# Kernel tuning notes

Hardware: AMD Instinct MI355X
Metric: run time of the kernel (lower is better)

## Reference

```python
import jax, jax.numpy as jnp
import numpy as np

N, F = 16384, 32
H1, H2, D1, D2 = 64, 64, 32, 1


def setup_inputs() -> dict:
    key = jax.random.key(0)
    ks = jax.random.split(key, 10)
    x = jax.random.normal(ks[0], (N, F), dtype=jnp.float32)
    # pre-normalized adjacency (GCNConv expects D^-1/2 A D^-1/2); mimic with uniform/N
    a = jax.random.uniform(ks[1], (N, N), dtype=jnp.float32) / N
    # glorot-ish scaled params
    W1 = jax.random.normal(ks[2], (F, H1), dtype=jnp.float32) * (1.0 / np.sqrt(F))
    b1 = jnp.zeros((H1,), dtype=jnp.float32)
    W2 = jax.random.normal(ks[3], (H1, H2), dtype=jnp.float32) * (1.0 / np.sqrt(H1))
    b2 = jnp.zeros((H2,), dtype=jnp.float32)
    Wd1 = jax.random.normal(ks[4], (H2, D1), dtype=jnp.float32) * (1.0 / np.sqrt(H2))
    bd1 = jnp.zeros((D1,), dtype=jnp.float32)
    Wd2 = jax.random.normal(ks[5], (D1, D2), dtype=jnp.float32) * (1.0 / np.sqrt(D1))
    bd2 = jnp.zeros((D2,), dtype=jnp.float32)
    return {"x": x, "a": a, "W1": W1, "b1": b1, "W2": W2, "b2": b2,
            "Wd1": Wd1, "bd1": bd1, "Wd2": Wd2, "bd2": bd2}


def reference(x, a, W1, b1, W2, b2, Wd1, bd1, Wd2, bd2):
    # GCNConv: relu(a @ (x @ W) + b)   (a is pre-normalized)
    g1 = jax.nn.relu(a @ (x @ W1) + b1)   # [N, 64]
    g2 = jax.nn.relu(a @ (g1 @ W2) + b2)  # [N, 64]
    d3 = jax.nn.relu(g2 @ Wd1 + bd1)      # [N, 32]
    return d3 @ Wd2 + bd2                 # [N, 1]
```

## Files before the change

kernel.cpp:

```cpp
#include <hip/hip_runtime.h>
#include <hip/hip_bf16.h>


typedef __bf16 bf16x8 __attribute__((ext_vector_type(8)));
typedef float  f32x16 __attribute__((ext_vector_type(16)));
typedef float  f32x4v __attribute__((ext_vector_type(4)));
typedef int    i32x4  __attribute__((ext_vector_type(4)));

#define NNODE 16384
#define KDIM  16384
#define HCOL  64

__device__ inline i32x4 pack8(f32x4v a, f32x4v b){
  bf16x8 t;
  t[0]=(__bf16)a[0]; t[1]=(__bf16)a[1]; t[2]=(__bf16)a[2]; t[3]=(__bf16)a[3];
  t[4]=(__bf16)b[0]; t[5]=(__bf16)b[1]; t[6]=(__bf16)b[2]; t[7]=(__bf16)b[3];
  return __builtin_bit_cast(i32x4, t);
}
#define BC(x) __builtin_bit_cast(bf16x8, x)

__global__ __launch_bounds__(256, 1) void gcn_layer_kernel(
    const float* __restrict__ A,
    const __bf16* __restrict__ Ht,
    const float* __restrict__ bias,
    float* __restrict__ G)
{
  __shared__ i32x4 sA[4*2*512];
  __shared__ i32x4 sH[4*2*512];

  const int tid  = threadIdx.x;
  const int lane = tid & 63;
  const int kw   = tid >> 6;
  const int row0 = blockIdx.x * 64;

  const int rA0  = lane >> 3;
  const int ccA  = lane & 7;
  const int swzA = ccA ^ rA0;
  const int r    = lane & 31;
  const int hsub = lane >> 5;
  const int xs   = r & 7;

  const size_t k0 = (size_t)kw * 4096;

  f32x4v ra[16]; i32x4 rh[8];

  const float* pA0 = A + (size_t)(row0 + rA0) * KDIM + k0 + (size_t)ccA*8;
  const i32x4* pH0 = (const i32x4*)Ht + (size_t)rA0 * (KDIM/8) + k0/8 + ccA;

  auto stage_load = [&](int t){
    const float* pA = pA0 + (size_t)t*64;
    #pragma unroll
    for (int pi=0; pi<8; ++pi){
      const float* p = pA + (size_t)pi*8*KDIM;
      ra[2*pi]   = *(const f32x4v*)p;
      ra[2*pi+1] = *(const f32x4v*)(p+4);
    }
    const i32x4* pH = pH0 + (size_t)t*8;
    #pragma unroll
    for (int pi=0; pi<8; ++pi)
      rh[pi] = pH[(size_t)pi*8*(KDIM/8)];
  };

  auto stage_write = [&](int buf){
    i32x4* dA = &sA[(kw*2+buf)*512];
    #pragma unroll
    for (int pi=0; pi<8; ++pi)
      dA[(rA0 + pi*8)*8 + swzA] = pack8(ra[2*pi], ra[2*pi+1]);
    i32x4* dH = &sH[(kw*2+buf)*512];
    #pragma unroll
    for (int pi=0; pi<8; ++pi)
      dH[(rA0 + pi*8)*8 + swzA] = rh[pi];
  };

  f32x16 acc00 = {}, acc01 = {}, acc10 = {}, acc11 = {};

  auto compute = [&](int buf){
    const i32x4* bA = &sA[(kw*2+buf)*512];
    const i32x4* bH = &sH[(kw*2+buf)*512];
    #pragma unroll
    for (int kk=0; kk<4; ++kk){
      int c = (kk*2 + hsub) ^ xs;
      bf16x8 a0 = BC(bA[r*8 + c]);
      bf16x8 a1 = BC(bA[(r+32)*8 + c]);
      bf16x8 b0 = BC(bH[r*8 + c]);
      bf16x8 b1 = BC(bH[(r+32)*8 + c]);
      acc00 = __builtin_amdgcn_mfma_f32_32x32x16_bf16(a0, b0, acc00, 0,0,0);
      acc01 = __builtin_amdgcn_mfma_f32_32x32x16_bf16(a0, b1, acc01, 0,0,0);
      acc10 = __builtin_amdgcn_mfma_f32_32x32x16_bf16(a1, b0, acc10, 0,0,0);
      acc11 = __builtin_amdgcn_mfma_f32_32x32x16_bf16(a1, b1, acc11, 0,0,0);
    }
  };

  stage_load(0);
  stage_write(0);
  stage_load(1);
  #pragma unroll 1
  for (int t=0; t<63; ++t){
    compute(t&1);
    stage_write((t+1)&1);
    if (t < 62) stage_load(t+2);
  }
  compute(1);

  __syncthreads();

  float* red = (float*)sA;
  if (kw > 0){
    float* rd = red + (size_t)(kw-1)*4096;
    #pragma unroll
    for (int j=0; j<16; ++j){
      int rr = (j&3) + 8*(j>>2) + 4*hsub;
      rd[(rr   )*64 + r]      = acc00[j];
      rd[(rr   )*64 + 32 + r] = acc01[j];
      rd[(rr+32)*64 + r]      = acc10[j];
      rd[(rr+32)*64 + 32 + r] = acc11[j];
    }
  }
  __syncthreads();
  if (kw == 0){
    #pragma unroll
    for (int j=0; j<16; ++j){
      int rr = (j&3) + 8*(j>>2) + 4*hsub;
      float v00 = acc00[j] + red[(rr   )*64+r]    + red[4096+(rr   )*64+r]    + red[8192+(rr   )*64+r]    + bias[r];
      float v01 = acc01[j] + red[(rr   )*64+32+r] + red[4096+(rr   )*64+32+r] + red[8192+(rr   )*64+32+r] + bias[32+r];
      float v10 = acc10[j] + red[(rr+32)*64+r]    + red[4096+(rr+32)*64+r]    + red[8192+(rr+32)*64+r]    + bias[r];
      float v11 = acc11[j] + red[(rr+32)*64+32+r] + red[4096+(rr+32)*64+32+r] + red[8192+(rr+32)*64+32+r] + bias[32+r];
      G[(size_t)(row0 + rr     )*HCOL + r]      = fmaxf(v00, 0.f);
      G[(size_t)(row0 + rr     )*HCOL + 32 + r] = fmaxf(v01, 0.f);
      G[(size_t)(row0 + rr + 32)*HCOL + r]      = fmaxf(v10, 0.f);
      G[(size_t)(row0 + rr + 32)*HCOL + 32 + r] = fmaxf(v11, 0.f);
    }
  }
}

template<int F>
__global__ __launch_bounds__(128) void proj_T_kernel(
    const float* __restrict__ in,
    const float* __restrict__ W,
    __bf16* __restrict__ out)
{
  constexpr int FP = F + 4;
  __shared__ float sWt[64*FP];
  __shared__ short sOut[64*136];

  int tid = threadIdx.x;
  for (int e = tid; e < 64*F; e += 128){
    int h = e / F, j = e - h*F;
    sWt[h*FP + j] = W[j*64 + h];
  }
  __syncthreads();

  const size_t n = (size_t)blockIdx.x*128 + tid;
  float rowv[F];
  #pragma unroll
  for (int j=0; j<F; j+=4){
    f32x4v v = *(const f32x4v*)(in + n*F + j);
    rowv[j]=v[0]; rowv[j+1]=v[1]; rowv[j+2]=v[2]; rowv[j+3]=v[3];
  }
  #pragma unroll
  for (int h=0; h<64; ++h){
    float s = 0.f;
    #pragma unroll
    for (int j=0; j<F; j+=4){
      f32x4v w = *(const f32x4v*)&sWt[h*FP + j];
      s += rowv[j]*w[0] + rowv[j+1]*w[1] + rowv[j+2]*w[2] + rowv[j+3]*w[3];
    }
    sOut[h*136 + tid] = __builtin_bit_cast(short, (__bf16)s);
  }
  __syncthreads();

  const size_t n0 = (size_t)blockIdx.x*128;
  #pragma unroll
  for (int pi=0; pi<8; ++pi){
    int p = pi*128 + tid;
    int h = p >> 4, cc = p & 15;
    i32x4 v = *(const i32x4*)&sOut[h*136 + cc*8];
    *(i32x4*)(out + (size_t)h*NNODE + n0 + cc*8) = v;
  }
}

__global__ __launch_bounds__(256) void tail_kernel(
    const float* __restrict__ g2,
    const float* __restrict__ Wd1,
    const float* __restrict__ bd1,
    const float* __restrict__ Wd2,
    const float* __restrict__ bd2,
    float* __restrict__ outp)
{
  __shared__ float sW[64*32];
  __shared__ float sb1[32], sw2[32];
  int tid = threadIdx.x;
  for (int e=tid; e<2048; e+=256) sW[e] = Wd1[e];
  if (tid < 32){ sb1[tid] = bd1[tid]; sw2[tid] = Wd2[tid]; }
  __syncthreads();

  size_t n = (size_t)blockIdx.x*256 + tid;
  float rv[64];
  #pragma unroll
  for (int j=0;j<64;j+=4){
    f32x4v v = *(const f32x4v*)(g2 + n*64 + j);
    rv[j]=v[0]; rv[j+1]=v[1]; rv[j+2]=v[2]; rv[j+3]=v[3];
  }
  float o = 0.f;
  #pragma unroll
  for (int c=0;c<32;++c){
    float s = sb1[c];
    #pragma unroll
    for (int j=0;j<64;++j) s += rv[j]*sW[j*32 + c];
    o += fmaxf(s, 0.f) * sw2[c];
  }
  outp[n] = o + bd2[0];
}

extern "C" void kernel_launch(void* const* d_in, const int* in_sizes, int n_in,
                              void* d_out, int out_size, void* d_ws, size_t ws_size,
                              hipStream_t stream)
{
  const float* x   = (const float*)d_in[0];
  const float* a   = (const float*)d_in[1];
  const float* W1  = (const float*)d_in[2];
  const float* b1  = (const float*)d_in[3];
  const float* W2  = (const float*)d_in[4];
  const float* b2  = (const float*)d_in[5];
  const float* Wd1 = (const float*)d_in[6];
  const float* bd1 = (const float*)d_in[7];
  const float* Wd2 = (const float*)d_in[8];
  const float* bd2 = (const float*)d_in[9];
  float* outp = (float*)d_out;

  char* ws = (char*)d_ws;
  __bf16* Ht1 = (__bf16*)(ws);
  __bf16* Ht2 = (__bf16*)(ws + (2u<<20));
  float*  g1  = (float*)(ws + (4u<<20));
  float*  g2  = (float*)(ws + (8u<<20));

  proj_T_kernel<32><<<128, 128, 0, stream>>>(x,  W1, Ht1);
  gcn_layer_kernel <<<256, 256, 0, stream>>>(a, Ht1, b1, g1);
  proj_T_kernel<64><<<128, 128, 0, stream>>>(g1, W2, Ht2);
  gcn_layer_kernel <<<256, 256, 0, stream>>>(a, Ht2, b2, g2);
  tail_kernel      <<<64, 256, 0, stream>>>(g2, Wd1, bd1, Wd2, bd2, outp);
}
```

Measured before the change: 426.3 us.

## Load B operand directly into registers, drop its LDS staging, allow 2 blocks/CU

The projected-feature operand Ht is now read straight from global memory into registers in the MFMA operand layout, with a double-buffered register set, instead of being staged through shared memory. This halves the LDS footprint and the LDS write/read traffic per tile. Launch bounds now allow two blocks per CU for more occupancy. The cost is more VGPRs and uncoalesced-ish per-lane global loads of Ht, which is small and mostly cache-resident.

```diff
diff --git a/kernel.cpp b/kernel.cpp
--- a/kernel.cpp
+++ b/kernel.cpp
@@ -19,14 +19,13 @@
 }
 #define BC(x) __builtin_bit_cast(bf16x8, x)
 
-__global__ __launch_bounds__(256, 1) void gcn_layer_kernel(
+__global__ __launch_bounds__(256, 2) void gcn_layer_kernel(
     const float* __restrict__ A,
     const __bf16* __restrict__ Ht,
     const float* __restrict__ bias,
     float* __restrict__ G)
 {
   __shared__ i32x4 sA[4*2*512];
-  __shared__ i32x4 sH[4*2*512];
 
   const int tid  = threadIdx.x;
   const int lane = tid & 63;
@@ -42,12 +41,14 @@
 
   const size_t k0 = (size_t)kw * 4096;
 
-  f32x4v ra[16]; i32x4 rh[8];
-
-  const float* pA0 = A + (size_t)(row0 + rA0) * KDIM + k0 + (size_t)ccA*8;
-  const i32x4* pH0 = (const i32x4*)Ht + (size_t)rA0 * (KDIM/8) + k0/8 + ccA;
-
-  auto stage_load = [&](int t){
+  f32x4v ra[16];
+  i32x4  b0a[4], b1a[4], b0b[4], b1b[4];
+
+  const float*  pA0 = A  + (size_t)(row0 + rA0) * KDIM + k0 + (size_t)ccA*8;
+  const __bf16* pB0 = Ht + (size_t)r        * KDIM + k0 + (size_t)hsub*8;
+  const __bf16* pB1 = pB0 + (size_t)32 * KDIM;
+
+  auto loadA = [&](int t){
     const float* pA = pA0 + (size_t)t*64;
     #pragma unroll
     for (int pi=0; pi<8; ++pi){
@@ -55,52 +56,56 @@
       ra[2*pi]   = *(const f32x4v*)p;
       ra[2*pi+1] = *(const f32x4v*)(p+4);
     }
-    const i32x4* pH = pH0 + (size_t)t*8;
-    #pragma unroll
-    for (int pi=0; pi<8; ++pi)
-      rh[pi] = pH[(size_t)pi*8*(KDIM/8)];
-  };
-
-  auto stage_write = [&](int buf){
+  };
+  auto loadB = [&](i32x4 (&b0)[4], i32x4 (&b1)[4], int t){
+    const __bf16* q0 = pB0 + (size_t)t*64;
+    const __bf16* q1 = pB1 + (size_t)t*64;
+    #pragma unroll
+    for (int kk=0; kk<4; ++kk){
+      b0[kk] = *(const i32x4*)(q0 + kk*16);
+      b1[kk] = *(const i32x4*)(q1 + kk*16);
+    }
+  };
+  auto writeA = [&](int buf){
     i32x4* dA = &sA[(kw*2+buf)*512];
     #pragma unroll
     for (int pi=0; pi<8; ++pi)
       dA[(rA0 + pi*8)*8 + swzA] = pack8(ra[2*pi], ra[2*pi+1]);
-    i32x4* dH = &sH[(kw*2+buf)*512];
-    #pragma unroll
-    for (int pi=0; pi<8; ++pi)
-      dH[(rA0 + pi*8)*8 + swzA] = rh[pi];
   };
 
   f32x16 acc00 = {}, acc01 = {}, acc10 = {}, acc11 = {};
 
-  auto compute = [&](int buf){
+  auto compute = [&](int buf, i32x4 (&b0)[4], i32x4 (&b1)[4]){
     const i32x4* bA = &sA[(kw*2+buf)*512];
-    const i32x4* bH = &sH[(kw*2+buf)*512];
     #pragma unroll
     for (int kk=0; kk<4; ++kk){
       int c = (kk*2 + hsub) ^ xs;
       bf16x8 a0 = BC(bA[r*8 + c]);
       bf16x8 a1 = BC(bA[(r+32)*8 + c]);
-      bf16x8 b0 = BC(bH[r*8 + c]);
-      bf16x8 b1 = BC(bH[(r+32)*8 + c]);
-      acc00 = __builtin_amdgcn_mfma_f32_32x32x16_bf16(a0, b0, acc00, 0,0,0);
-      acc01 = __builtin_amdgcn_mfma_f32_32x32x16_bf16(a0, b1, acc01, 0,0,0);
-      acc10 = __builtin_amdgcn_mfma_f32_32x32x16_bf16(a1, b0, acc10, 0,0,0);
-      acc11 = __builtin_amdgcn_mfma_f32_32x32x16_bf16(a1, b1, acc11, 0,0,0);
-    }
-  };
-
-  stage_load(0);
-  stage_write(0);
-  stage_load(1);
+      acc00 = __builtin_amdgcn_mfma_f32_32x32x16_bf16(a0, BC(b0[kk]), acc00, 0,0,0);
+      acc01 = __builtin_amdgcn_mfma_f32_32x32x16_bf16(a0, BC(b1[kk]), acc01, 0,0,0);
+      acc10 = __builtin_amdgcn_mfma_f32_32x32x16_bf16(a1, BC(b0[kk]), acc10, 0,0,0);
+      acc11 = __builtin_amdgcn_mfma_f32_32x32x16_bf16(a1, BC(b1[kk]), acc11, 0,0,0);
+    }
+  };
+
+  loadA(0); loadB(b0a, b1a, 0);
+  writeA(0);
+  loadA(1); loadB(b0b, b1b, 1);
   #pragma unroll 1
-  for (int t=0; t<63; ++t){
-    compute(t&1);
-    stage_write((t+1)&1);
-    if (t < 62) stage_load(t+2);
-  }
-  compute(1);
+  for (int t=0; t<62; t+=2){
+    compute(0, b0a, b1a);
+    loadB(b0a, b1a, t+2);
+    writeA(1);
+    loadA(t+2);
+    compute(1, b0b, b1b);
+    loadB(b0b, b1b, t+3);
+    writeA(0);
+    loadA(t+3);
+  }
+  compute(0, b0a, b1a);
+  writeA(1);
+  compute(1, b0b, b1b);
 
   __syncthreads();
 
```

Result: slower. 1.474 ms (+245.7%).
